# Kernel optimization log

Hardware: AMD Instinct MI355X
Metric: run time of the kernel (lower is better)

Reference implementation:

```python
import jax, jax.numpy as jnp
import numpy as np

L, V, P, D, H, F = 6, 50257, 1024, 1024, 16, 4096
DH = D // H
EPS = 1e-5


def setup_inputs() -> dict:
    key = jax.random.key(0)
    ks = jax.random.split(key, 8)
    s = 0.02  # init scale to keep activations sane across layers
    inp = {
        "input_ids": jax.random.randint(ks[0], (2, 1024), 0, V),
        "wte": jax.random.normal(ks[1], (V, D), jnp.float32) * s,
        "wpe": jax.random.normal(ks[2], (P, D), jnp.float32) * s,
        "ln1_g": jnp.ones((L, D), jnp.float32),
        "ln1_b": jnp.zeros((L, D), jnp.float32),
        "wq": jax.random.normal(ks[3], (L, D, D), jnp.float32) * s,
        "bq": jnp.zeros((L, D), jnp.float32),
        "wk": jax.random.normal(ks[4], (L, D, D), jnp.float32) * s,
        "bk": jnp.zeros((L, D), jnp.float32),
        "wv": jax.random.normal(ks[5], (L, D, D), jnp.float32) * s,
        "bv": jnp.zeros((L, D), jnp.float32),
        "wo": jax.random.normal(jax.random.fold_in(key, 10), (L, D, D), jnp.float32) * s,
        "bo": jnp.zeros((L, D), jnp.float32),
        "ln2_g": jnp.ones((L, D), jnp.float32),
        "ln2_b": jnp.zeros((L, D), jnp.float32),
        "w1": jax.random.normal(ks[6], (L, D, F), jnp.float32) * s,
        "b1": jnp.zeros((L, F), jnp.float32),
        "w2": jax.random.normal(ks[7], (L, F, D), jnp.float32) * s,
        "b2": jnp.zeros((L, D), jnp.float32),
        "lnf_g": jnp.ones((D,), jnp.float32),
        "lnf_b": jnp.zeros((D,), jnp.float32),
    }
    return inp


def _ln(x, g, b):
    m = jnp.mean(x, axis=-1, keepdims=True)
    v = jnp.mean(jnp.square(x - m), axis=-1, keepdims=True)
    return (x - m) * jax.lax.rsqrt(v + EPS) * g + b


def _block(x, p):
    (g1, be1, wq, bq, wk, bk, wv, bv, wo, bo, g2, be2, w1, b1, w2, b2) = p
    B, T, _ = x.shape
    h = _ln(x, g1, be1)
    q = (h @ wq + bq).reshape(B, T, H, DH)
    k = (h @ wk + bk).reshape(B, T, H, DH)
    v = (h @ wv + bv).reshape(B, T, H, DH)
    scores = jnp.einsum("bqhd,bkhd->bhqk", q, k) * (1.0 / np.sqrt(DH))
    attn = jax.nn.softmax(scores, axis=-1)  # NOTE: no causal mask (as in source)
    o = jnp.einsum("bhqk,bkhd->bqhd", attn, v).reshape(B, T, D)
    x = x + o @ wo + bo
    h2 = _ln(x, g2, be2)
    x = x + jax.nn.gelu(h2 @ w1 + b1, approximate=False) @ w2 + b2
    return x


def reference(input_ids, wte, wpe, ln1_g, ln1_b, wq, bq, wk, bk, wv, bv,
              wo, bo, ln2_g, ln2_b, w1, b1, w2, b2, lnf_g, lnf_b):
    T = input_ids.shape[1]
    x = wte[input_ids] + wpe[:T]  # [B,T,D]
    params = (ln1_g, ln1_b, wq, bq, wk, bk, wv, bv, wo, bo,
              ln2_g, ln2_b, w1, b1, w2, b2)

    def step(x, p):
        return _block(x, p), None

    x, _ = jax.lax.scan(step, x, params)
    return _ln(x, lnf_g, lnf_b)
```

## Files before the change

kernel.cpp:

```cpp
#include <hip/hip_runtime.h>
#include <hip/hip_bf16.h>
#include <math.h>

#define DV 1024
#define FF 4096
#define NLAY 6
#define NH 16
#define TT 1024
#define NTOK 2048

typedef float f32x4 __attribute__((ext_vector_type(4)));
typedef short bf16x8 __attribute__((ext_vector_type(8)));
typedef unsigned short u16;
typedef u16 u16x4 __attribute__((ext_vector_type(4)));
typedef u16 u16x8 __attribute__((ext_vector_type(8)));

__device__ __forceinline__ u16 f2b(float f) {
  unsigned u = __float_as_uint(f);
  unsigned r = (u + 0x7fffu + ((u >> 16) & 1u)) >> 16;
  return (u16)r;
}
__device__ __forceinline__ float b2f(u16 u) {
  return __uint_as_float(((unsigned)u) << 16);
}

__device__ __forceinline__ void gload_lds16(const void* g, void* lds) {
  __builtin_amdgcn_global_load_lds(
      (const __attribute__((address_space(1))) void*)g,
      (__attribute__((address_space(3))) void*)lds, 16, 0, 0);
}

__global__ __launch_bounds__(256) void embed_ln_k(const int* __restrict__ ids,
                                                  const float* __restrict__ wte,
                                                  const float* __restrict__ wpe,
                                                  const float* __restrict__ gg,
                                                  const float* __restrict__ bb,
                                                  float* __restrict__ X,
                                                  u16* __restrict__ outb) {
  int row = blockIdx.x, tid = threadIdx.x;
  int t = row & (TT - 1);
  int id = ids[row];
  f32x4 a = *(const f32x4*)(wte + (size_t)id * DV + tid * 4);
  f32x4 p = *(const f32x4*)(wpe + (size_t)t * DV + tid * 4);
  f32x4 v = a + p;
  *(f32x4*)(X + (size_t)row * DV + tid * 4) = v;
  float s1 = v[0] + v[1] + v[2] + v[3];
  float s2 = v[0] * v[0] + v[1] * v[1] + v[2] * v[2] + v[3] * v[3];
#pragma unroll
  for (int o = 32; o >= 1; o >>= 1) {
    s1 += __shfl_xor(s1, o);
    s2 += __shfl_xor(s2, o);
  }
  __shared__ float sh[8];
  int w = tid >> 6;
  if ((tid & 63) == 0) { sh[w] = s1; sh[w + 4] = s2; }
  __syncthreads();
  s1 = sh[0] + sh[1] + sh[2] + sh[3];
  s2 = sh[4] + sh[5] + sh[6] + sh[7];
  float mean = s1 * (1.0f / DV);
  float var = s2 * (1.0f / DV) - mean * mean;
  float rstd = rsqrtf(var + 1e-5f);
  f32x4 gv = *(const f32x4*)(gg + tid * 4);
  f32x4 bv = *(const f32x4*)(bb + tid * 4);
  u16x4 r;
#pragma unroll
  for (int i = 0; i < 4; ++i) r[i] = f2b((v[i] - mean) * rstd * gv[i] + bv[i]);
  *(u16x4*)(outb + (size_t)row * DV + tid * 4) = r;
}

template <int OUTF>
__global__ __launch_bounds__(256) void ln_k(const float* __restrict__ X,
                                            const float* __restrict__ gg,
                                            const float* __restrict__ bb,
                                            u16* __restrict__ outb,
                                            float* __restrict__ outf) {
  int row = blockIdx.x, tid = threadIdx.x;
  f32x4 v = *(const f32x4*)(X + (size_t)row * DV + tid * 4);
  float s1 = v[0] + v[1] + v[2] + v[3];
  float s2 = v[0] * v[0] + v[1] * v[1] + v[2] * v[2] + v[3] * v[3];
#pragma unroll
  for (int o = 32; o >= 1; o >>= 1) {
    s1 += __shfl_xor(s1, o);
    s2 += __shfl_xor(s2, o);
  }
  __shared__ float sh[8];
  int w = tid >> 6;
  if ((tid & 63) == 0) { sh[w] = s1; sh[w + 4] = s2; }
  __syncthreads();
  s1 = sh[0] + sh[1] + sh[2] + sh[3];
  s2 = sh[4] + sh[5] + sh[6] + sh[7];
  float mean = s1 * (1.0f / DV);
  float var = s2 * (1.0f / DV) - mean * mean;
  float rstd = rsqrtf(var + 1e-5f);
  f32x4 gv = *(const f32x4*)(gg + tid * 4);
  f32x4 bv = *(const f32x4*)(bb + tid * 4);
  f32x4 o;
#pragma unroll
  for (int i = 0; i < 4; ++i) o[i] = (v[i] - mean) * rstd * gv[i] + bv[i];
  if (OUTF) {
    *(f32x4*)(outf + (size_t)row * DV + tid * 4) = o;
  } else {
    u16x4 r = {f2b(o[0]), f2b(o[1]), f2b(o[2]), f2b(o[3])};
    *(u16x4*)(outb + (size_t)row * DV + tid * 4) = r;
  }
}

template <int NS, int OUTF>
__global__ __launch_bounds__(256) void reduce_ln_k(
    float* __restrict__ X, const u16* __restrict__ pp,
    const float* __restrict__ bias, const float* __restrict__ gg,
    const float* __restrict__ bb, u16* __restrict__ outb,
    float* __restrict__ outf) {
  int row = blockIdx.x, tid = threadIdx.x;
  size_t off = (size_t)row * DV + tid * 4;
  f32x4 v = *(const f32x4*)(X + off);
  if (NS > 0) {
    f32x4 bvv = *(const f32x4*)(bias + tid * 4);
    v += bvv;
#pragma unroll
    for (int s = 0; s < NS; ++s) {
      u16x4 pv = *(const u16x4*)(pp + (size_t)s * NTOK * DV + off);
      v[0] += b2f(pv[0]); v[1] += b2f(pv[1]);
      v[2] += b2f(pv[2]); v[3] += b2f(pv[3]);
    }
    *(f32x4*)(X + off) = v;
  }
  float s1 = v[0] + v[1] + v[2] + v[3];
  float s2 = v[0] * v[0] + v[1] * v[1] + v[2] * v[2] + v[3] * v[3];
#pragma unroll
  for (int o = 32; o >= 1; o >>= 1) {
    s1 += __shfl_xor(s1, o);
    s2 += __shfl_xor(s2, o);
  }
  __shared__ float sh[8];
  int w = tid >> 6;
  if ((tid & 63) == 0) { sh[w] = s1; sh[w + 4] = s2; }
  __syncthreads();
  s1 = sh[0] + sh[1] + sh[2] + sh[3];
  s2 = sh[4] + sh[5] + sh[6] + sh[7];
  float mean = s1 * (1.0f / DV);
  float var = s2 * (1.0f / DV) - mean * mean;
  float rstd = rsqrtf(var + 1e-5f);
  f32x4 gv = *(const f32x4*)(gg + tid * 4);
  f32x4 bv = *(const f32x4*)(bb + tid * 4);
  f32x4 o;
#pragma unroll
  for (int i = 0; i < 4; ++i) o[i] = (v[i] - mean) * rstd * gv[i] + bv[i];
  if (OUTF) {
    *(f32x4*)(outf + off) = o;
  } else {
    u16x4 r = {f2b(o[0]), f2b(o[1]), f2b(o[2]), f2b(o[3])};
    *(u16x4*)(outb + off) = r;
  }
}

__global__ __launch_bounds__(256) void transw_k(const float* __restrict__ wq,
                                                const float* __restrict__ wk,
                                                const float* __restrict__ wv,
                                                const float* __restrict__ wo,
                                                const float* __restrict__ w1,
                                                const float* __restrict__ w2,
                                                u16* __restrict__ WT) {
  int lay = blockIdx.y;
  size_t oDD = (size_t)lay * DV * DV, oDF = (size_t)lay * DV * FF;
  u16* WTL = WT + (size_t)lay * 12 * 1024 * 1024;
  int b0 = blockIdx.x;
  int bid = (b0 & 7) * 96 + (b0 >> 3);
  const float* src;
  u16* dst;
  int K, N, tile;
  if (bid < 256) {
    int which = bid >> 6;
    src = (which == 0 ? wq : which == 1 ? wk : which == 2 ? wv : wo) + oDD;
    dst = WTL + (size_t)which * (DV * DV);
    K = DV; N = DV; tile = bid & 63;
  } else if (bid < 512) {
    src = w1 + oDF; dst = WTL + (size_t)4 * (DV * DV); K = DV; N = FF; tile = bid - 256;
  } else {
    src = w2 + oDF; dst = WTL + (size_t)8 * (DV * DV); K = FF; N = DV; tile = bid - 512;
  }
  int ntc = N >> 7;
  int tr = tile / ntc, tc = tile - tr * ntc;
  int k0 = tr * 128, n0 = tc * 128;
  __shared__ u16 ts[128][130];
  int tid = threadIdx.x;
  int lr = tid >> 5, lc = (tid & 31) * 4;
  f32x4 vv[16];
#pragma unroll
  for (int p = 0; p < 16; ++p)
    vv[p] = *(const f32x4*)(src + (size_t)(k0 + p * 8 + lr) * N + n0 + lc);
#pragma unroll
  for (int p = 0; p < 16; ++p) {
    int k = p * 8 + lr;
    ts[k][lc + 0] = f2b(vv[p][0]);
    ts[k][lc + 1] = f2b(vv[p][1]);
    ts[k][lc + 2] = f2b(vv[p][2]);
    ts[k][lc + 3] = f2b(vv[p][3]);
  }
  __syncthreads();
  int m = tid & 15, u2 = tid >> 4;
#pragma unroll
  for (int p = 0; p < 8; ++p) {
    int n = p * 16 + u2;
#pragma unroll
    for (int s = 0; s < 2; ++s) {
      int kk = s * 64 + m * 4;
      u16x4 ov = {ts[kk][n], ts[kk + 1][n], ts[kk + 2][n], ts[kk + 3][n]};
      *(u16x4*)(dst + (size_t)(n0 + n) * K + k0 + kk) = ov;
    }
  }
}

template <int EPI>
__global__ __launch_bounds__(256) void gemm_k(
    const u16* __restrict__ A, const u16* __restrict__ Wt,
    const float* __restrict__ b0, const float* __restrict__ b1,
    u16* __restrict__ o0, u16* __restrict__ o1,
    u16* __restrict__ o2t, u16* __restrict__ op, float* __restrict__ of,
    const float* __restrict__ res, int M, int N, int K, int KS) {
  int z = blockIdx.z;
  const u16* W = Wt;
  const float* bias = b0;
  u16* outb = o0;
  if (EPI == 0) {
    W = Wt + (size_t)z * N * K;
    bias = z == 0 ? b0 : b1;
    outb = z == 0 ? o0 : o1;
  }
  int kbeg = (EPI == 3) ? z * KS : 0;
  int klen = (EPI == 3) ? KS : K;
  int bm = blockIdx.x * 128, bn = blockIdx.y * 128;
  __shared__ __attribute__((aligned(16))) u16 SM[32768];
  u16* As = SM;
  u16* Bs = SM + 16384;
  u16* Cs = SM;
  int tid = threadIdx.x, l = tid & 63, w = tid >> 6;
  int q = l & 15, g = l >> 4;
  int wm = (w >> 1) * 64, wn = (w & 1) * 64;
  int srow = w * 32 + (l >> 3);
  int scol = (((l & 7) ^ ((l >> 3) & 7))) * 8;
  const u16* Ab = A + (size_t)(bm + srow) * K + kbeg + scol;
  const u16* Wb = W + (size_t)(bn + srow) * K + kbeg + scol;
  f32x4 acc[4][4] = {};
  int nk = klen >> 6;
#pragma unroll
  for (int i = 0; i < 4; ++i) {
    gload_lds16(Ab + (size_t)i * 8 * K, &As[(w * 32 + i * 8) * 64]);
    gload_lds16(Wb + (size_t)i * 8 * K, &Bs[(w * 32 + i * 8) * 64]);
  }
  __syncthreads();
  for (int t = 0; t < nk; ++t) {
    int cur = t & 1;
    if (t + 1 < nk) {
      int ko = (t + 1) * 64;
#pragma unroll
      for (int i = 0; i < 4; ++i) {
        gload_lds16(Ab + (size_t)i * 8 * K + ko,
                    &As[(cur ^ 1) * 8192 + (w * 32 + i * 8) * 64]);
        gload_lds16(Wb + (size_t)i * 8 * K + ko,
                    &Bs[(cur ^ 1) * 8192 + (w * 32 + i * 8) * 64]);
      }
    }
#pragma unroll
    for (int kk = 0; kk < 2; ++kk) {
      bf16x8 af[4], bfr[4];
#pragma unroll
      for (int f = 0; f < 4; ++f) {
        int ra = wm + f * 16 + q, rb = wn + f * 16 + q;
        af[f]  = *(const bf16x8*)(&As[cur * 8192 + ra * 64 + ((kk * 4 + g) ^ (ra & 7)) * 8]);
        bfr[f] = *(const bf16x8*)(&Bs[cur * 8192 + rb * 64 + ((kk * 4 + g) ^ (rb & 7)) * 8]);
      }
#pragma unroll
      for (int fm = 0; fm < 4; ++fm)
#pragma unroll
        for (int fn = 0; fn < 4; ++fn)
          acc[fm][fn] = __builtin_amdgcn_mfma_f32_16x16x32_bf16(af[fm], bfr[fn],
                                                                acc[fm][fn], 0, 0, 0);
    }
    __syncthreads();
  }
  if (EPI == 2) {
#pragma unroll
    for (int fm = 0; fm < 4; ++fm)
#pragma unroll
      for (int fn = 0; fn < 4; ++fn) {
        int gcol = bn + wn + fn * 16 + q;
        int growb = bm + wm + fm * 16 + g * 4;
        float bv = bias[gcol];
#pragma unroll
        for (int r = 0; r < 4; ++r)
          of[(size_t)(growb + r) * N + gcol] = res[(size_t)(growb + r) * N + gcol]
                                               + acc[fm][fn][r] + bv;
      }
    return;
  }
#pragma unroll
  for (int fm = 0; fm < 4; ++fm) {
#pragma unroll
    for (int fn = 0; fn < 4; ++fn) {
      int cL = wn + fn * 16 + q;
      float bv = (EPI == 3) ? 0.0f : bias[bn + cL];
#pragma unroll
      for (int r = 0; r < 4; ++r) {
        int rL = wm + fm * 16 + g * 4 + r;
        float v = acc[fm][fn][r] + bv;
        if (EPI == 1) v = 0.5f * v * (1.0f + erff(v * 0.70710678118f));
        if (EPI == 4) Cs[cL * 132 + rL] = f2b(v);
        else          Cs[rL * 132 + cL] = f2b(v);
      }
    }
  }
  __syncthreads();
  {
    int rowL = tid >> 4, c8 = (tid & 15) * 8;
#pragma unroll
    for (int p = 0; p < 8; ++p) {
      int row = p * 16 + rowL;
      u16x4 lo = *(const u16x4*)(&Cs[row * 132 + c8]);
      u16x4 hi = *(const u16x4*)(&Cs[row * 132 + c8 + 4]);
      u16x8 ov = {lo[0], lo[1], lo[2], lo[3], hi[0], hi[1], hi[2], hi[3]};
      if (EPI == 4) {
        *(u16x8*)(o2t + (size_t)(bn + row) * M + bm + c8) = ov;
      } else if (EPI == 3) {
        *(u16x8*)(op + (size_t)z * M * N + (size_t)(bm + row) * N + bn + c8) = ov;
      } else {
        *(u16x8*)(outb + (size_t)(bm + row) * N + bn + c8) = ov;
      }
    }
  }
}

__global__ __launch_bounds__(256) void attn_k(const u16* __restrict__ Q,
                                              const u16* __restrict__ Kb,
                                              const u16* __restrict__ Vt,
                                              u16* __restrict__ O) {
  int bid = blockIdx.x;
  int qt = bid & 15, h = (bid >> 4) & 15, b = bid >> 8;
  int tid = threadIdx.x, l = tid & 63, w = tid >> 6;
  int q = l & 15, g = l >> 4;
  int tokbase = b * TT;
  int qbase = tokbase + qt * 64 + w * 16;
  __shared__ __attribute__((aligned(16))) u16 Ks[2][32 * 64];
  __shared__ __attribute__((aligned(16))) u16 Vs[2][64 * 32];
  __shared__ __attribute__((aligned(16))) u16 Ps[4][512];
  bf16x8 qf[2];
  {
    int qrow = qbase + q;
#pragma unroll
    for (int half = 0; half < 2; ++half)
      qf[half] = *(const bf16x8*)(Q + (size_t)qrow * DV + h * 64 + half * 32 + g * 8);
  }
  int key_s = w * 8 + (l >> 3), c_s = l & 7;
  const u16* ksrc = Kb + (size_t)(tokbase + key_s) * DV + h * 64 + ((c_s ^ (key_s & 7)) * 8);
  int dl = w * 16 + (l >> 2), c2 = l & 3;
  const u16* vsrc = Vt + (size_t)(h * 64 + dl) * NTOK + tokbase + ((c2 ^ (dl & 3)) * 8);
  f32x4 oacc[4] = {};
  float m_run = -INFINITY, l_run = 0.0f;
  gload_lds16(ksrc, &Ks[0][w * 512]);
  gload_lds16(vsrc, &Vs[0][w * 512]);
  __syncthreads();
  for (int kbk = 0; kbk < TT / 32; ++kbk) {
    int cur = kbk & 1;
    if (kbk + 1 < TT / 32) {
      gload_lds16(ksrc + (size_t)(kbk + 1) * 32 * DV, &Ks[cur ^ 1][w * 512]);
      gload_lds16(vsrc + (kbk + 1) * 32, &Vs[cur ^ 1][w * 512]);
    }
    f32x4 s[2] = {};
#pragma unroll
    for (int kt = 0; kt < 2; ++kt)
#pragma unroll
      for (int half = 0; half < 2; ++half) {
        int row = kt * 16 + q;
        int chunk = (half * 4 + g) ^ (row & 7);
        bf16x8 kf = *(const bf16x8*)(&Ks[cur][row * 64 + chunk * 8]);
        s[kt] = __builtin_amdgcn_mfma_f32_16x16x32_bf16(kf, qf[half], s[kt], 0, 0, 0);
      }
    float tmax = -INFINITY;
#pragma unroll
    for (int kt = 0; kt < 2; ++kt)
#pragma unroll
      for (int r = 0; r < 4; ++r) {
        s[kt][r] *= 0.125f;
        tmax = fmaxf(tmax, s[kt][r]);
      }
    tmax = fmaxf(tmax, __shfl_xor(tmax, 16));
    tmax = fmaxf(tmax, __shfl_xor(tmax, 32));
    float m_new = fmaxf(m_run, tmax);
    float corr = __expf(m_run - m_new);
    float psum = 0.0f;
    u16 pb[2][4];
#pragma unroll
    for (int kt = 0; kt < 2; ++kt)
#pragma unroll
      for (int r = 0; r < 4; ++r) {
        float p = __expf(s[kt][r] - m_new);
        psum += p;
        pb[kt][r] = f2b(p);
      }
    psum += __shfl_xor(psum, 16);
    psum += __shfl_xor(psum, 32);
    l_run = l_run * corr + psum;
    m_run = m_new;
#pragma unroll
    for (int kt = 0; kt < 2; ++kt) {
      u16x4 pv4 = {pb[kt][0], pb[kt][1], pb[kt][2], pb[kt][3]};
      *(u16x4*)(&Ps[w][q * 32 + ((kt * 4 + g) ^ (q & 7)) * 4]) = pv4;
    }
    float corr4[4];
#pragma unroll
    for (int r = 0; r < 4; ++r) corr4[r] = __shfl(corr, g * 4 + r);
#pragma unroll
    for (int nt = 0; nt < 4; ++nt)
#pragma unroll
      for (int r = 0; r < 4; ++r) oacc[nt][r] *= corr4[r];
    u16x4 a0 = *(const u16x4*)(&Ps[w][q * 32 + ((2 * g) ^ (q & 7)) * 4]);
    u16x4 a1 = *(const u16x4*)(&Ps[w][q * 32 + ((2 * g + 1) ^ (q & 7)) * 4]);
    bf16x8 pa = {(short)a0[0], (short)a0[1], (short)a0[2], (short)a0[3],
                 (short)a1[0], (short)a1[1], (short)a1[2], (short)a1[3]};
#pragma unroll
    for (int nt = 0; nt < 4; ++nt) {
      int vrow = nt * 16 + q;
      int vc = g ^ (vrow & 3);
      bf16x8 vf = *(const bf16x8*)(&Vs[cur][vrow * 32 + vc * 8]);
      oacc[nt] = __builtin_amdgcn_mfma_f32_16x16x32_bf16(pa, vf, oacc[nt], 0, 0, 0);
    }
    __syncthreads();
  }
  float rl[4];
#pragma unroll
  for (int r = 0; r < 4; ++r) rl[r] = 1.0f / __shfl(l_run, g * 4 + r);
#pragma unroll
  for (int nt = 0; nt < 4; ++nt)
#pragma unroll
    for (int r = 0; r < 4; ++r) {
      int qrw = qbase + g * 4 + r;
      int d = nt * 16 + q;
      O[(size_t)qrw * DV + h * 64 + d] = f2b(oacc[nt][r] * rl[r]);
    }
}

extern "C" void kernel_launch(void* const* d_in, const int* in_sizes, int n_in,
                              void* d_out, int out_size, void* d_ws, size_t ws_size,
                              hipStream_t stream) {
  const int*   ids = (const int*)d_in[0];
  const float* wte = (const float*)d_in[1];
  const float* wpe = (const float*)d_in[2];
  const float* l1g = (const float*)d_in[3];
  const float* l1b = (const float*)d_in[4];
  const float* wq  = (const float*)d_in[5];
  const float* bq  = (const float*)d_in[6];
  const float* wk  = (const float*)d_in[7];
  const float* bk  = (const float*)d_in[8];
  const float* wv  = (const float*)d_in[9];
  const float* bv  = (const float*)d_in[10];
  const float* wo  = (const float*)d_in[11];
  const float* bo  = (const float*)d_in[12];
  const float* l2g = (const float*)d_in[13];
  const float* l2b = (const float*)d_in[14];
  const float* w1  = (const float*)d_in[15];
  const float* b1  = (const float*)d_in[16];
  const float* w2  = (const float*)d_in[17];
  const float* b2  = (const float*)d_in[18];
  const float* lfg = (const float*)d_in[19];
  const float* lfb = (const float*)d_in[20];
  (void)in_sizes; (void)n_in; (void)out_size;

  bool bigws = ws_size >= ((size_t)221 << 20);
  bool midws = ws_size >= ((size_t)101 << 20);

  char* ws = (char*)d_ws;
  float* x   = (float*)(ws + 0);
  u16*   hb  = (u16*)(ws + ((size_t)8 << 20));
  u16*   qb  = (u16*)(ws + ((size_t)12 << 20));
  u16*   kb  = (u16*)(ws + ((size_t)16 << 20));
  u16*   vbt = (u16*)(ws + ((size_t)20 << 20));
  u16*   ab  = (u16*)(ws + ((size_t)24 << 20));
  u16*   mb  = (u16*)(ws + ((size_t)28 << 20));
  u16*   pp  = (u16*)(ws + ((size_t)44 << 20));
  u16*   WT  = (u16*)(ws + ((size_t)(midws ? 76 : 44) << 20));

  if (bigws)
    transw_k<<<dim3(768, 6), 256, 0, stream>>>(wq, wk, wv, wo, w1, w2, WT);
  embed_ln_k<<<NTOK, 256, 0, stream>>>(ids, wte, wpe, l1g, l1b, x, hb);

  for (int lay = 0; lay < NLAY; ++lay) {
    size_t oDD = (size_t)lay * DV * DV;
    size_t oDF = (size_t)lay * DV * FF;
    u16* WTL = bigws ? WT + (size_t)lay * 12 * 1024 * 1024 : WT;
    if (!bigws)
      transw_k<<<dim3(768, 1), 256, 0, stream>>>(wq + oDD, wk + oDD, wv + oDD,
                                                 wo + oDD, w1 + oDF, w2 + oDF, WTL);
    gemm_k<0><<<dim3(16, 8, 2), 256, 0, stream>>>(
        hb, WTL, bq + lay * DV, bk + lay * DV,
        qb, kb, nullptr, nullptr, nullptr, nullptr, NTOK, DV, DV, 0);
    gemm_k<4><<<dim3(16, 8, 1), 256, 0, stream>>>(
        hb, WTL + (size_t)2 * DV * DV, bv + lay * DV, nullptr,
        nullptr, nullptr, vbt, nullptr, nullptr, nullptr, NTOK, DV, DV, 0);
    attn_k<<<512, 256, 0, stream>>>(qb, kb, vbt, ab);
    if (midws) {
      gemm_k<3><<<dim3(16, 8, 2), 256, 0, stream>>>(
          ab, WTL + (size_t)3 * DV * DV, nullptr, nullptr,
          nullptr, nullptr, nullptr, pp, nullptr, nullptr, NTOK, DV, DV, 512);
      reduce_ln_k<2, 0><<<NTOK, 256, 0, stream>>>(
          x, pp, bo + lay * DV, l2g + lay * DV, l2b + lay * DV, hb, nullptr);
    } else {
      gemm_k<2><<<dim3(16, 8, 1), 256, 0, stream>>>(
          ab, WTL + (size_t)3 * DV * DV, bo + lay * DV, nullptr,
          nullptr, nullptr, nullptr, nullptr, x, x, NTOK, DV, DV, 0);
      ln_k<0><<<NTOK, 256, 0, stream>>>(x, l2g + lay * DV, l2b + lay * DV, hb, nullptr);
    }
    gemm_k<1><<<dim3(16, 32, 1), 256, 0, stream>>>(
        hb, WTL + (size_t)4 * DV * DV, b1 + lay * FF, nullptr,
        mb, nullptr, nullptr, nullptr, nullptr, nullptr, NTOK, FF, DV, 0);
    if (midws) {
      gemm_k<3><<<dim3(16, 8, 4), 256, 0, stream>>>(
          mb, WTL + (size_t)8 * DV * DV, nullptr, nullptr,
          nullptr, nullptr, nullptr, pp, nullptr, nullptr, NTOK, DV, FF, 1024);
      if (lay < NLAY - 1)
        reduce_ln_k<4, 0><<<NTOK, 256, 0, stream>>>(
            x, pp, b2 + lay * DV, l1g + (lay + 1) * DV, l1b + (lay + 1) * DV,
            hb, nullptr);
      else
        reduce_ln_k<4, 1><<<NTOK, 256, 0, stream>>>(
            x, pp, b2 + lay * DV, lfg, lfb, nullptr, (float*)d_out);
    } else {
      gemm_k<2><<<dim3(16, 8, 1), 256, 0, stream>>>(
          mb, WTL + (size_t)8 * DV * DV, b2 + lay * DV, nullptr,
          nullptr, nullptr, nullptr, nullptr, x, x, NTOK, DV, FF, 0);
      if (lay < NLAY - 1)
        ln_k<0><<<NTOK, 256, 0, stream>>>(x, l1g + (lay + 1) * DV,
                                          l1b + (lay + 1) * DV, hb, nullptr);
      else
        ln_k<1><<<NTOK, 256, 0, stream>>>(x, lfg, lfb, nullptr, (float*)d_out);
    }
  }
}
```

Before: 1.007 ms.

## Fuse QKV projections into one launch, swizzle GEMM tiles, retile weight transpose

Merges the separate Q/K and transposed-V GEMM launches into a single three-slice launch, with the V slice selecting the transposed epilogue at runtime. Adds an XCD-aware block swizzle to all GEMM launches so neighbouring tiles land on the same chiplet for L2 reuse. Rewrites the weight-transpose kernel to use 64x256 tiles with vectorised LDS writes and 16-byte global stores, and removes its previous block swizzle. The runtime transposed-store branch adds a little divergence-free overhead to every GEMM epilogue.

```diff
diff --git a/kernel.cpp b/kernel.cpp
--- a/kernel.cpp
+++ b/kernel.cpp
@@ -164,8 +164,7 @@
   int lay = blockIdx.y;
   size_t oDD = (size_t)lay * DV * DV, oDF = (size_t)lay * DV * FF;
   u16* WTL = WT + (size_t)lay * 12 * 1024 * 1024;
-  int b0 = blockIdx.x;
-  int bid = (b0 & 7) * 96 + (b0 >> 3);
+  int bid = blockIdx.x;
   const float* src;
   u16* dst;
   int K, N, tile;
@@ -179,35 +178,29 @@
   } else {
     src = w2 + oDF; dst = WTL + (size_t)8 * (DV * DV); K = FF; N = DV; tile = bid - 512;
   }
-  int ntc = N >> 7;
+  int ntc = N >> 8;
   int tr = tile / ntc, tc = tile - tr * ntc;
-  int k0 = tr * 128, n0 = tc * 128;
-  __shared__ u16 ts[128][130];
-  int tid = threadIdx.x;
-  int lr = tid >> 5, lc = (tid & 31) * 4;
+  int k0 = tr * 64, n0 = tc * 256;
+  __shared__ u16 ts[64][258];
+  int tid = threadIdx.x, l = tid & 63, w = tid >> 6;
   f32x4 vv[16];
 #pragma unroll
-  for (int p = 0; p < 16; ++p)
-    vv[p] = *(const f32x4*)(src + (size_t)(k0 + p * 8 + lr) * N + n0 + lc);
-#pragma unroll
-  for (int p = 0; p < 16; ++p) {
-    int k = p * 8 + lr;
-    ts[k][lc + 0] = f2b(vv[p][0]);
-    ts[k][lc + 1] = f2b(vv[p][1]);
-    ts[k][lc + 2] = f2b(vv[p][2]);
-    ts[k][lc + 3] = f2b(vv[p][3]);
-  }
-  __syncthreads();
-  int m = tid & 15, u2 = tid >> 4;
-#pragma unroll
-  for (int p = 0; p < 8; ++p) {
-    int n = p * 16 + u2;
-#pragma unroll
-    for (int s = 0; s < 2; ++s) {
-      int kk = s * 64 + m * 4;
-      u16x4 ov = {ts[kk][n], ts[kk + 1][n], ts[kk + 2][n], ts[kk + 3][n]};
-      *(u16x4*)(dst + (size_t)(n0 + n) * K + k0 + kk) = ov;
-    }
+  for (int i = 0; i < 16; ++i)
+    vv[i] = *(const f32x4*)(src + (size_t)(k0 + i * 4 + w) * N + n0 + l * 4);
+#pragma unroll
+  for (int i = 0; i < 16; ++i) {
+    u16x4 c = {f2b(vv[i][0]), f2b(vv[i][1]), f2b(vv[i][2]), f2b(vv[i][3])};
+    *(u16x4*)(&ts[i * 4 + w][l * 4]) = c;
+  }
+  __syncthreads();
+  int kk = (tid & 7) * 8, nn = tid >> 3;
+#pragma unroll
+  for (int j = 0; j < 8; ++j) {
+    int n = j * 32 + nn;
+    u16x8 ov;
+#pragma unroll
+    for (int m = 0; m < 8; ++m) ov[m] = ts[kk + m][n];
+    *(u16x8*)(dst + (size_t)(n0 + n) * K + k0 + kk) = ov;
   }
 }
 
@@ -215,7 +208,7 @@
 __global__ __launch_bounds__(256) void gemm_k(
     const u16* __restrict__ A, const u16* __restrict__ Wt,
     const float* __restrict__ b0, const float* __restrict__ b1,
-    u16* __restrict__ o0, u16* __restrict__ o1,
+    const float* __restrict__ b2v, u16* __restrict__ o0, u16* __restrict__ o1,
     u16* __restrict__ o2t, u16* __restrict__ op, float* __restrict__ of,
     const float* __restrict__ res, int M, int N, int K, int KS) {
   int z = blockIdx.z;
@@ -224,12 +217,16 @@
   u16* outb = o0;
   if (EPI == 0) {
     W = Wt + (size_t)z * N * K;
-    bias = z == 0 ? b0 : b1;
+    bias = z == 0 ? b0 : z == 1 ? b1 : b2v;
     outb = z == 0 ? o0 : o1;
   }
+  int gx = gridDim.x, nwg = gx * gridDim.y;
+  int lin = blockIdx.y * gx + blockIdx.x;
+  int cpx = nwg >> 3;
+  int swz = (lin & 7) * cpx + (lin >> 3);
+  int bm = (swz % gx) * 128, bn = (swz / gx) * 128;
   int kbeg = (EPI == 3) ? z * KS : 0;
   int klen = (EPI == 3) ? KS : K;
-  int bm = blockIdx.x * 128, bn = blockIdx.y * 128;
   __shared__ __attribute__((aligned(16))) u16 SM[32768];
   u16* As = SM;
   u16* Bs = SM + 16384;
@@ -294,6 +291,7 @@
       }
     return;
   }
+  bool tr = (EPI == 0 && z == 2);
 #pragma unroll
   for (int fm = 0; fm < 4; ++fm) {
 #pragma unroll
@@ -305,8 +303,8 @@
         int rL = wm + fm * 16 + g * 4 + r;
         float v = acc[fm][fn][r] + bv;
         if (EPI == 1) v = 0.5f * v * (1.0f + erff(v * 0.70710678118f));
-        if (EPI == 4) Cs[cL * 132 + rL] = f2b(v);
-        else          Cs[rL * 132 + cL] = f2b(v);
+        if (tr) Cs[cL * 132 + rL] = f2b(v);
+        else    Cs[rL * 132 + cL] = f2b(v);
       }
     }
   }
@@ -319,7 +317,7 @@
       u16x4 lo = *(const u16x4*)(&Cs[row * 132 + c8]);
       u16x4 hi = *(const u16x4*)(&Cs[row * 132 + c8 + 4]);
       u16x8 ov = {lo[0], lo[1], lo[2], lo[3], hi[0], hi[1], hi[2], hi[3]};
-      if (EPI == 4) {
+      if (tr) {
         *(u16x8*)(o2t + (size_t)(bn + row) * M + bm + c8) = ov;
       } else if (EPI == 3) {
         *(u16x8*)(op + (size_t)z * M * N + (size_t)(bm + row) * N + bn + c8) = ov;
@@ -490,31 +488,28 @@
     if (!bigws)
       transw_k<<<dim3(768, 1), 256, 0, stream>>>(wq + oDD, wk + oDD, wv + oDD,
                                                  wo + oDD, w1 + oDF, w2 + oDF, WTL);
-    gemm_k<0><<<dim3(16, 8, 2), 256, 0, stream>>>(
-        hb, WTL, bq + lay * DV, bk + lay * DV,
-        qb, kb, nullptr, nullptr, nullptr, nullptr, NTOK, DV, DV, 0);
-    gemm_k<4><<<dim3(16, 8, 1), 256, 0, stream>>>(
-        hb, WTL + (size_t)2 * DV * DV, bv + lay * DV, nullptr,
-        nullptr, nullptr, vbt, nullptr, nullptr, nullptr, NTOK, DV, DV, 0);
+    gemm_k<0><<<dim3(16, 8, 3), 256, 0, stream>>>(
+        hb, WTL, bq + lay * DV, bk + lay * DV, bv + lay * DV,
+        qb, kb, vbt, nullptr, nullptr, nullptr, NTOK, DV, DV, 0);
     attn_k<<<512, 256, 0, stream>>>(qb, kb, vbt, ab);
     if (midws) {
       gemm_k<3><<<dim3(16, 8, 2), 256, 0, stream>>>(
-          ab, WTL + (size_t)3 * DV * DV, nullptr, nullptr,
+          ab, WTL + (size_t)3 * DV * DV, nullptr, nullptr, nullptr,
           nullptr, nullptr, nullptr, pp, nullptr, nullptr, NTOK, DV, DV, 512);
       reduce_ln_k<2, 0><<<NTOK, 256, 0, stream>>>(
           x, pp, bo + lay * DV, l2g + lay * DV, l2b + lay * DV, hb, nullptr);
     } else {
       gemm_k<2><<<dim3(16, 8, 1), 256, 0, stream>>>(
-          ab, WTL + (size_t)3 * DV * DV, bo + lay * DV, nullptr,
+          ab, WTL + (size_t)3 * DV * DV, bo + lay * DV, nullptr, nullptr,
           nullptr, nullptr, nullptr, nullptr, x, x, NTOK, DV, DV, 0);
       ln_k<0><<<NTOK, 256, 0, stream>>>(x, l2g + lay * DV, l2b + lay * DV, hb, nullptr);
     }
     gemm_k<1><<<dim3(16, 32, 1), 256, 0, stream>>>(
-        hb, WTL + (size_t)4 * DV * DV, b1 + lay * FF, nullptr,
+        hb, WTL + (size_t)4 * DV * DV, b1 + lay * FF, nullptr, nullptr,
         mb, nullptr, nullptr, nullptr, nullptr, nullptr, NTOK, FF, DV, 0);
     if (midws) {
       gemm_k<3><<<dim3(16, 8, 4), 256, 0, stream>>>(
-          mb, WTL + (size_t)8 * DV * DV, nullptr, nullptr,
+          mb, WTL + (size_t)8 * DV * DV, nullptr, nullptr, nullptr,
           nullptr, nullptr, nullptr, pp, nullptr, nullptr, NTOK, DV, FF, 1024);
       if (lay < NLAY - 1)
         reduce_ln_k<4, 0><<<NTOK, 256, 0, stream>>>(
@@ -525,7 +520,7 @@
             x, pp, b2 + lay * DV, lfg, lfb, nullptr, (float*)d_out);
     } else {
       gemm_k<2><<<dim3(16, 8, 1), 256, 0, stream>>>(
-          mb, WTL + (size_t)8 * DV * DV, b2 + lay * DV, nullptr,
+          mb, WTL + (size_t)8 * DV * DV, b2 + lay * DV, nullptr, nullptr,
           nullptr, nullptr, nullptr, nullptr, x, x, NTOK, DV, FF, 0);
       if (lay < NLAY - 1)
         ln_k<0><<<NTOK, 256, 0, stream>>>(x, l1g + (lay + 1) * DV,
```

Measured after the change: 946.0 us. -6.0%, faster.
